# Kernel tuning notes

Measured on AMD Instinct MI355X. Metric: run time of the kernel, lower is better.

Reference implementation:

```python
import jax, jax.numpy as jnp
import numpy as np

NH = 8  # num_heads
CHUNK = 32  # query-block size for chunked L1 cdist


def _mlp(x, w1, b1, w2, b2, w3, b3):
    h = jax.nn.relu(x @ w1 + b1)
    h = jax.nn.relu(h @ w2 + b2)
    return h @ w3 + b3


def _split_heads(x, nh):
    # Faithful to source: reshape last dim as (d, nh) then permute -> [B, nh, S, d]
    B, S, H = x.shape
    return jnp.transpose(x.reshape(B, S, H // nh, nh), (0, 3, 1, 2))


def _cdist_l1(K, Q, chunk=CHUNK):
    # torch.cdist(K, Q, p=1): D[b,h,i,j] = sum_d |K[b,h,i,d] - Q[b,h,j,d]|
    # Chunk over query rows to bound the broadcasted |K-Q| intermediate.
    B, h, Sq, d = Q.shape
    Sk = K.shape[2]
    Qb = jnp.moveaxis(Q.reshape(B, h, Sq // chunk, chunk, d), 2, 0)  # [nb,B,h,chunk,d]

    def block(q):  # q: [B,h,chunk,d]
        return jnp.sum(jnp.abs(K[:, :, :, None, :] - q[:, :, None, :, :]), axis=-1)  # [B,h,Sk,chunk]

    D = jax.lax.map(block, Qb)  # [nb,B,h,Sk,chunk]
    return jnp.moveaxis(D, 0, 3).reshape(B, h, Sk, Sq)


def setup_inputs() -> dict:
    key = jax.random.key(0)
    ks = jax.random.split(key, 32)
    B, S, F, H, O = 4, 1024, 128, 512, 128
    s = 0.02

    def lin(i, fin, fout):
        return (jax.random.normal(ks[i], (fin, fout), jnp.float32) * s,
                jnp.zeros((fout,), jnp.float32))

    inp = {
        'KEY': jax.random.normal(ks[0], (B, S, F), jnp.float32),
        'VALUE': jax.random.normal(ks[1], (B, S, F), jnp.float32),
        'QUERY': jax.random.normal(ks[2], (B, S, F), jnp.float32),
    }
    idx = 3
    for n in ['k', 'q', 'v']:
        for li, (fin, fout) in enumerate([(F, H), (H, H), (H, H)], 1):
            w, b = lin(idx, fin, fout); idx += 1
            inp[f'W{n}_w{li}'] = w
            inp[f'W{n}_b{li}'] = b
    w, b = lin(idx, H, O)
    inp['Wo_w'] = w
    inp['Wo_b'] = b
    return inp


def reference(KEY, VALUE, QUERY,
              Wk_w1, Wk_b1, Wk_w2, Wk_b2, Wk_w3, Wk_b3,
              Wq_w1, Wq_b1, Wq_w2, Wq_b2, Wq_w3, Wq_b3,
              Wv_w1, Wv_b1, Wv_w2, Wv_b2, Wv_w3, Wv_b3,
              Wo_w, Wo_b):
    Wk = _split_heads(_mlp(KEY, Wk_w1, Wk_b1, Wk_w2, Wk_b2, Wk_w3, Wk_b3), NH)   # [B,h,Sk,d]
    Wq = _split_heads(_mlp(QUERY, Wq_w1, Wq_b1, Wq_w2, Wq_b2, Wq_w3, Wq_b3), NH)  # [B,h,Sq,d]
    Wv = _split_heads(_mlp(VALUE, Wv_w1, Wv_b1, Wv_w2, Wv_b2, Wv_w3, Wv_b3), NH)  # [B,h,Sk,d]

    D = _cdist_l1(Wk, Wq)                              # [B,h,Sk,Sq]
    attn = jax.nn.softmax(-(D * D) * 0.5, axis=1)      # softmax over HEAD axis, as in source
    out = jnp.einsum('bhik,bhij->bhjk', attn, Wv)      # [B,h,d,Sq]
    B, h, d, Sq = out.shape
    out = jnp.transpose(out, (0, 2, 1, 3)).reshape(B, d * h, Sq)  # [B,hidden,Sq]
    out = jnp.transpose(out, (0, 2, 1))                # [B,Sq,hidden]
    return out @ Wo_w + Wo_b                           # dropout = identity (eval)
```

## Files before the change

kernel.cpp:

```cpp
#include <hip/hip_runtime.h>
#include <hip/hip_bf16.h>
#include <hip/hip_fp16.h>

typedef unsigned short u16;
typedef __attribute__((ext_vector_type(8))) short short8;
typedef __attribute__((ext_vector_type(4))) float floatx4;

#define DEVI static __device__ __forceinline__

DEVI float bf2f(u16 b) { return __uint_as_float(((unsigned)b) << 16); }
DEVI u16 f2bf(float f) {
  __hip_bfloat16 h = __float2bfloat16(f);
  u16 u; __builtin_memcpy(&u, &h, 2); return u;
}
DEVI u16 f2h(float f) {
  __half h = __float2half(f);
  u16 u; __builtin_memcpy(&u, &h, 2); return u;
}

DEVI void async_ld16(const u16* g, u16* l) {
  __builtin_amdgcn_global_load_lds(
      (const __attribute__((address_space(1))) unsigned int*)g,
      (__attribute__((address_space(3))) unsigned int*)l, 16, 0, 0);
}

template <int CTRL>
DEVI float dpp_add_f(float v) {
  int i; __builtin_memcpy(&i, &v, 4);
  int p = __builtin_amdgcn_update_dpp(0, i, CTRL, 0xF, 0xF, false);
  float pv; __builtin_memcpy(&pv, &p, 4);
  return v + pv;
}

DEVI int hperm(int f) { return ((f & 7) << 6) | (f >> 3); }

struct H4 { __half2 a, b, c, d; };
DEVI H4 toH4(const int4 v) { H4 r; __builtin_memcpy(&r, &v, 16); return r; }
DEVI int4 fromH4(const H4 x) { int4 r; __builtin_memcpy(&r, &x, 16); return r; }

struct TransArgs {
  const float* src[10];
  u16* dst[10];
  int R[10];
  int C[10];
};

__global__ __launch_bounds__(256) void transpose_k(TransArgs t) {
  const int z = blockIdx.z;
  const float* __restrict__ src = t.src[z];
  u16* __restrict__ dst = t.dst[z];
  const int R = t.R[z], C = t.C[z];
  const int c0 = blockIdx.x * 32, r0 = blockIdx.y * 32;
  if (c0 >= C || r0 >= R) return;
  __shared__ float tile[32][33];
  const int tx = threadIdx.x & 31, ty = threadIdx.x >> 5;
  for (int i = ty; i < 32; i += 8)
    tile[i][tx] = src[(size_t)(r0 + i) * C + c0 + tx];
  __syncthreads();
  for (int i = ty; i < 32; i += 8) {
    const int f = r0 + tx;
    const int fi = (z == 9) ? hperm(f) : f;
    dst[(size_t)(c0 + i) * R + fi] = f2bf(tile[tx][i]);
  }
}

struct ConvArgs {
  const float* src[3];
  u16* dst[3];
};

__global__ __launch_bounds__(256) void conv_k(ConvArgs c) {
  const int z = blockIdx.z;
  const float* __restrict__ src = c.src[z];
  u16* __restrict__ dst = c.dst[z];
  const size_t i = ((size_t)blockIdx.x * 256 + threadIdx.x) * 8;
  const float4 f0 = *(const float4*)(src + i);
  const float4 f1 = *(const float4*)(src + i + 4);
  u16 tmp[8] = {f2bf(f0.x), f2bf(f0.y), f2bf(f0.z), f2bf(f0.w),
                f2bf(f1.x), f2bf(f1.y), f2bf(f1.z), f2bf(f1.w)};
  int4 t; __builtin_memcpy(&t, tmp, 16);
  *(int4*)(dst + i) = t;
}

struct GemmArgs {
  const u16* A[3];
  const u16* WT[3];
  const float* bias[3];
  void* C[3];
};

__global__ __launch_bounds__(256, 3) void gemm128(GemmArgs ga, int M, int N, int K,
                                                  int relu, int c_mode, int out_perm) {
  const int z = blockIdx.z;
  const u16* __restrict__ A = ga.A[z];
  const u16* __restrict__ WT = ga.WT[z];
  const float* __restrict__ bias = ga.bias[z];
  void* __restrict__ C = ga.C[z];

  __shared__ u16 As[128 * 64];
  __shared__ u16 Bs[128 * 64];

  const int tid = threadIdx.x;
  const int lane = tid & 63;
  const int wave = tid >> 6;
  const int wm = wave >> 1, wn = wave & 1;
  const int mb = blockIdx.y, nb = blockIdx.x;

  floatx4 acc[4][4];
#pragma unroll
  for (int mi = 0; mi < 4; ++mi)
#pragma unroll
    for (int ni = 0; ni < 4; ++ni) acc[mi][ni] = floatx4{0.f, 0.f, 0.f, 0.f};

  const int g = (lane & 7) ^ ((lane >> 3) & 7);
  const int srow = lane >> 3;
  const size_t aRowBase = (size_t)(mb * 128 + wave * 32 + srow) * K + g * 8;
  const size_t bRowBase = (size_t)(nb * 128 + wave * 32 + srow) * K + g * 8;

  for (int k0 = 0; k0 < K; k0 += 64) {
    __syncthreads();
#pragma unroll
    for (int it = 0; it < 4; ++it) {
      async_ld16(A + aRowBase + (size_t)it * 8 * K + k0, As + (wave * 32 + it * 8) * 64);
      async_ld16(WT + bRowBase + (size_t)it * 8 * K + k0, Bs + (wave * 32 + it * 8) * 64);
    }
    __syncthreads();
#pragma unroll
    for (int ks = 0; ks < 2; ++ks) {
      const int phys = ((ks * 4 + (lane >> 4)) ^ (lane & 7)) * 8;
      short8 af[4], bf[4];
#pragma unroll
      for (int i = 0; i < 4; ++i) {
        const int m = wm * 64 + i * 16 + (lane & 15);
        const int n = wn * 64 + i * 16 + (lane & 15);
        af[i] = *(const short8*)(As + m * 64 + phys);
        bf[i] = *(const short8*)(Bs + n * 64 + phys);
      }
#pragma unroll
      for (int mi = 0; mi < 4; ++mi)
#pragma unroll
        for (int ni = 0; ni < 4; ++ni)
          acc[mi][ni] = __builtin_amdgcn_mfma_f32_16x16x32_bf16(af[mi], bf[ni], acc[mi][ni], 0, 0, 0);
    }
  }

#pragma unroll
  for (int mi = 0; mi < 4; ++mi)
#pragma unroll
    for (int ni = 0; ni < 4; ++ni) {
      const int col = nb * 128 + wn * 64 + ni * 16 + (lane & 15);
      const float bv = bias[col];
      const int colw = out_perm ? hperm(col) : col;
      const floatx4 v = acc[mi][ni];
#pragma unroll
      for (int r = 0; r < 4; ++r) {
        const int row = mb * 128 + wm * 64 + mi * 16 + (lane >> 4) * 4 + r;
        float x = v[r] + bv;
        if (relu) x = fmaxf(x, 0.f);
        if (c_mode == 1)      ((float*)C)[(size_t)row * N + colw] = x;
        else if (c_mode == 2) ((u16*)C)[(size_t)row * N + colw] = f2h(x);
        else                  ((u16*)C)[(size_t)row * N + colw] = f2bf(x);
      }
    }
}

__global__ __launch_bounds__(256, 3) void attn_kernel(const u16* __restrict__ Km,
                                                      const u16* __restrict__ Qm,
                                                      const u16* __restrict__ Vm,
                                                      u16* __restrict__ partial) {
  __shared__ alignas(16) u16 lds[4 * 4096];

  const int tid = threadIdx.x;
  const int lane = tid & 63;
  const int wave = tid >> 6;
  const int wid = blockIdx.x * 4 + wave;
  const int qt = wid & 63;
  const int sp = (wid >> 6) & 15;
  const int b = wid >> 10;
  const int j0 = qt * 16;

  const int qg = lane >> 4;
  const int h = (lane >> 1) & 7;
  const int half = lane & 1;

  int grans[4];
#pragma unroll
  for (int pi = 0; pi < 4; ++pi)
    grans[pi] = h * 8 + half * 4 + ((pi + h) & 3);

  H4 Qh[4][4];
#pragma unroll
  for (int qi = 0; qi < 4; ++qi) {
    const u16* qrow = Qm + (size_t)(b * 1024 + j0 + qg + qi * 4) * 512;
#pragma unroll
    for (int pi = 0; pi < 4; ++pi)
      Qh[qi][pi] = toH4(*(const int4*)(qrow + grans[pi] * 8));
  }

  const __half2 z2 = __float2half2_rn(0.f);
  H4 o[4][4];
#pragma unroll
  for (int qi = 0; qi < 4; ++qi)
#pragma unroll
    for (int pi = 0; pi < 4; ++pi) { o[qi][pi].a = z2; o[qi][pi].b = z2; o[qi][pi].c = z2; o[qi][pi].d = z2; }

  const int keyBase = b * 1024 + sp * 64;
  const u16* kgb = Km + (size_t)keyBase * 512 + lane * 8;
  const u16* vgb = Vm + (size_t)keyBase * 512 + lane * 8;
  u16* wbase = lds + wave * 4096;

  async_ld16(kgb, wbase);
  async_ld16(kgb + 512, wbase + 512);
  async_ld16(vgb, wbase + 1024);
  async_ld16(vgb + 512, wbase + 1536);

#pragma unroll 1
  for (int cc = 0; cc < 32; ++cc) {
    asm volatile("s_waitcnt vmcnt(0)" ::: "memory");
    __builtin_amdgcn_sched_barrier(0);
    const int cur = cc & 1;
    const u16* buf = wbase + cur * 2048;
    if (cc < 31) {
      const u16* kg = kgb + (size_t)(cc + 1) * 1024;
      const u16* vg = vgb + (size_t)(cc + 1) * 1024;
      u16* nb = wbase + (cur ^ 1) * 2048;
      async_ld16(kg, nb);
      async_ld16(kg + 512, nb + 512);
      async_ld16(vg, nb + 1024);
      async_ld16(vg + 512, nb + 1536);
    }

#pragma unroll
    for (int r = 0; r < 2; ++r) {
      const u16* krow = buf + r * 512;
      const u16* vrow = buf + 1024 + r * 512;

      __half2 a0[4], a1[4];
#pragma unroll
      for (int qi = 0; qi < 4; ++qi) { a0[qi] = z2; a1[qi] = z2; }
#pragma unroll
      for (int pi = 0; pi < 4; ++pi) {
        const H4 k4 = toH4(*(const int4*)(krow + grans[pi] * 8));
#pragma unroll
        for (int qi = 0; qi < 4; ++qi) {
          a0[qi] = __hadd2(a0[qi], __habs2(__hsub2(k4.a, Qh[qi][pi].a)));
          a1[qi] = __hadd2(a1[qi], __habs2(__hsub2(k4.b, Qh[qi][pi].b)));
          a0[qi] = __hadd2(a0[qi], __habs2(__hsub2(k4.c, Qh[qi][pi].c)));
          a1[qi] = __hadd2(a1[qi], __habs2(__hsub2(k4.d, Qh[qi][pi].d)));
        }
      }

      __half2 wh[4];
#pragma unroll
      for (int qi = 0; qi < 4; ++qi) {
        const __half2 s2 = __hadd2(a0[qi], a1[qi]);
        float d8p = __half2float(__low2half(s2)) + __half2float(__high2half(s2));
        const float d8 = dpp_add_f<0xB1>(d8p);
        const float e = __expf(-0.5f * d8 * d8);
        float nrm = e;
        nrm = dpp_add_f<0x4E>(nrm);
        nrm = dpp_add_f<0x141>(nrm);
        nrm = dpp_add_f<0x140>(nrm);
        const float w = e * __builtin_amdgcn_rcpf(nrm);
        wh[qi] = __float2half2_rn(w);
      }

#pragma unroll
      for (int pi = 0; pi < 4; ++pi) {
        const H4 v4 = toH4(*(const int4*)(vrow + grans[pi] * 8));
#pragma unroll
        for (int qi = 0; qi < 4; ++qi) {
          o[qi][pi].a = __hfma2(wh[qi], v4.a, o[qi][pi].a);
          o[qi][pi].b = __hfma2(wh[qi], v4.b, o[qi][pi].b);
          o[qi][pi].c = __hfma2(wh[qi], v4.c, o[qi][pi].c);
          o[qi][pi].d = __hfma2(wh[qi], v4.d, o[qi][pi].d);
        }
      }
    }
  }

  u16* Ew = wbase;
#pragma unroll
  for (int qi = 0; qi < 4; ++qi) {
#pragma unroll
    for (int pi = 0; pi < 4; ++pi)
      *(int4*)(Ew + qg * 512 + grans[pi] * 8) = fromH4(o[qi][pi]);
    asm volatile("s_waitcnt lgkmcnt(0)" ::: "memory");
#pragma unroll
    for (int p = 0; p < 4; ++p) {
      const int4 v = *(const int4*)(Ew + p * 512 + lane * 8);
      u16* dst = partial + (size_t)sp * (4096 * 512) + (size_t)(b * 1024 + j0 + p + qi * 4) * 512;
      *(int4*)(dst + lane * 8) = v;
    }
    asm volatile("s_waitcnt lgkmcnt(0)" ::: "memory");
  }
}

__global__ __launch_bounds__(256) void reduce_k(const u16* __restrict__ p,
                                                u16* __restrict__ out) {
  const size_t i = ((size_t)blockIdx.x * 256 + threadIdx.x) * 8;
  float s[8] = {0.f, 0.f, 0.f, 0.f, 0.f, 0.f, 0.f, 0.f};
#pragma unroll
  for (int sp = 0; sp < 16; ++sp) {
    const int4 t = *(const int4*)(p + (size_t)sp * (4096 * 512) + i);
    const __half* th = reinterpret_cast<const __half*>(&t);
#pragma unroll
    for (int j = 0; j < 8; ++j) s[j] += __half2float(th[j]);
  }
  int4 pk;
  u16* pu = reinterpret_cast<u16*>(&pk);
#pragma unroll
  for (int j = 0; j < 8; ++j) pu[j] = f2bf(s[j]);
  *(int4*)(out + i) = pk;
}

extern "C" void kernel_launch(void* const* d_in, const int* in_sizes, int n_in,
                              void* d_out, int out_size, void* d_ws, size_t ws_size,
                              hipStream_t stream) {
  (void)in_sizes; (void)n_in; (void)out_size; (void)ws_size;
  char* wsp = (char*)d_ws;
  size_t off = 0;
  auto take = [&](size_t bytes) {
    void* p = (void*)(wsp + off);
    off += ((bytes + 255) & ~(size_t)255);
    return p;
  };

  static const int wR[10] = {128, 512, 512, 128, 512, 512, 128, 512, 512, 512};
  static const int wC[10] = {512, 512, 512, 512, 512, 512, 512, 512, 512, 128};
  static const int widx[10] = {3, 5, 7, 9, 11, 13, 15, 17, 19, 21};

  u16* WT[10];
  for (int i = 0; i < 10; ++i) WT[i] = (u16*)take((size_t)wR[i] * wC[i] * 2);
  u16* a0[3]; for (int i = 0; i < 3; ++i) a0[i] = (u16*)take((size_t)4096 * 128 * 2);
  u16* h1[3]; for (int i = 0; i < 3; ++i) h1[i] = (u16*)take((size_t)4096 * 512 * 2);
  u16* h2[3]; for (int i = 0; i < 3; ++i) h2[i] = (u16*)take((size_t)4096 * 512 * 2);
  u16* partial = (u16*)take((size_t)16 * 4096 * 512 * 2);

  TransArgs ta;
  for (int i = 0; i < 10; ++i) {
    ta.src[i] = (const float*)d_in[widx[i]];
    ta.dst[i] = WT[i];
    ta.R[i] = wR[i];
    ta.C[i] = wC[i];
  }
  hipLaunchKernelGGL(transpose_k, dim3(16, 16, 10), dim3(256), 0, stream, ta);

  ConvArgs ca;
  ca.src[0] = (const float*)d_in[0]; ca.src[1] = (const float*)d_in[2]; ca.src[2] = (const float*)d_in[1];
  ca.dst[0] = a0[0]; ca.dst[1] = a0[1]; ca.dst[2] = a0[2];
  hipLaunchKernelGGL(conv_k, dim3(256, 1, 3), dim3(256), 0, stream, ca);

  GemmArgs g1 = {};
  for (int i = 0; i < 3; ++i) g1.A[i] = a0[i];
  g1.WT[0] = WT[0]; g1.WT[1] = WT[3]; g1.WT[2] = WT[6];
  g1.bias[0] = (const float*)d_in[4]; g1.bias[1] = (const float*)d_in[10]; g1.bias[2] = (const float*)d_in[16];
  g1.C[0] = h1[0]; g1.C[1] = h1[1]; g1.C[2] = h1[2];
  hipLaunchKernelGGL(gemm128, dim3(4, 32, 3), dim3(256), 0, stream, g1, 4096, 512, 128, 1, 0, 0);

  GemmArgs g2 = {};
  for (int i = 0; i < 3; ++i) { g2.A[i] = h1[i]; g2.C[i] = h2[i]; }
  g2.WT[0] = WT[1]; g2.WT[1] = WT[4]; g2.WT[2] = WT[7];
  g2.bias[0] = (const float*)d_in[6]; g2.bias[1] = (const float*)d_in[12]; g2.bias[2] = (const float*)d_in[18];
  hipLaunchKernelGGL(gemm128, dim3(4, 32, 3), dim3(256), 0, stream, g2, 4096, 512, 512, 1, 0, 0);

  GemmArgs g3 = {};
  for (int i = 0; i < 3; ++i) { g3.A[i] = h2[i]; g3.C[i] = (void*)h1[i]; }
  g3.WT[0] = WT[2]; g3.WT[1] = WT[5]; g3.WT[2] = WT[8];
  g3.bias[0] = (const float*)d_in[8]; g3.bias[1] = (const float*)d_in[14]; g3.bias[2] = (const float*)d_in[20];
  hipLaunchKernelGGL(gemm128, dim3(4, 32, 3), dim3(256), 0, stream, g3, 4096, 512, 512, 0, 2, 1);

  hipLaunchKernelGGL(attn_kernel, dim3(1024), dim3(256), 0, stream, h1[0], h1[1], h1[2], partial);

  hipLaunchKernelGGL(reduce_k, dim3(1024), dim3(256), 0, stream, partial, h2[0]);

  GemmArgs g4 = {};
  g4.A[0] = h2[0]; g4.WT[0] = WT[9]; g4.bias[0] = (const float*)d_in[22]; g4.C[0] = d_out;
  hipLaunchKernelGGL(gemm128, dim3(1, 32, 1), dim3(256), 0, stream, g4, 4096, 128, 512, 0, 1, 0);
}
```

Measured before the change: 357.4 us.

## Fuse split-K partial reduction into final output GEMM with atomic accumulation

The separate reduce kernel and the final 4096x512x128 GEMM are replaced by one kernel. Each block reduces the 16 fp16 partial slices for its 128x64 A-tile straight into LDS as bf16 and multiplies it against a 64-wide K chunk of the output weights. Results are accumulated into a zeroed fp32 output with atomicAdd across 8 K-chunks, and bias is added only by the first chunk. This removes the intermediate bf16 round trip through global memory and one launch, and spreads the final GEMM over 256 blocks instead of 32. In exchange it adds a memset, fp32 atomics on the output, and a summation order that is no longer deterministic.

```diff
diff --git a/kernel.cpp b/kernel.cpp
--- a/kernel.cpp
+++ b/kernel.cpp
@@ -296,22 +296,85 @@
   }
 }
 
-__global__ __launch_bounds__(256) void reduce_k(const u16* __restrict__ p,
-                                                u16* __restrict__ out) {
-  const size_t i = ((size_t)blockIdx.x * 256 + threadIdx.x) * 8;
-  float s[8] = {0.f, 0.f, 0.f, 0.f, 0.f, 0.f, 0.f, 0.f};
-#pragma unroll
-  for (int sp = 0; sp < 16; ++sp) {
-    const int4 t = *(const int4*)(p + (size_t)sp * (4096 * 512) + i);
-    const __half* th = reinterpret_cast<const __half*>(&t);
-#pragma unroll
-    for (int j = 0; j < 8; ++j) s[j] += __half2float(th[j]);
-  }
-  int4 pk;
-  u16* pu = reinterpret_cast<u16*>(&pk);
-#pragma unroll
-  for (int j = 0; j < 8; ++j) pu[j] = f2bf(s[j]);
-  *(int4*)(out + i) = pk;
+__global__ __launch_bounds__(256, 3) void gemm_final(const u16* __restrict__ P,
+                                                     const u16* __restrict__ WT9,
+                                                     const float* __restrict__ bias,
+                                                     float* __restrict__ out) {
+  __shared__ u16 As[128 * 64];
+  __shared__ u16 Bs[128 * 64];
+
+  const int tid = threadIdx.x;
+  const int lane = tid & 63;
+  const int wave = tid >> 6;
+  const int wm = wave >> 1, wn = wave & 1;
+  const int mb = blockIdx.y;
+  const int kc = blockIdx.x;
+  const int k0 = kc * 64;
+
+  const int g = (lane & 7) ^ ((lane >> 3) & 7);
+  const int srow = lane >> 3;
+
+  const size_t bRowBase = (size_t)(wave * 32 + srow) * 512 + g * 8;
+#pragma unroll
+  for (int it = 0; it < 4; ++it)
+    async_ld16(WT9 + bRowBase + (size_t)it * 8 * 512 + k0, Bs + (wave * 32 + it * 8) * 64);
+
+#pragma unroll
+  for (int it = 0; it < 4; ++it) {
+    const size_t gaddr = (size_t)(mb * 128 + wave * 32 + it * 8 + srow) * 512 + k0 + g * 8;
+    float s[8] = {0.f, 0.f, 0.f, 0.f, 0.f, 0.f, 0.f, 0.f};
+#pragma unroll
+    for (int sp = 0; sp < 16; ++sp) {
+      const int4 t = *(const int4*)(P + (size_t)sp * (4096 * 512) + gaddr);
+      const __half* th = reinterpret_cast<const __half*>(&t);
+#pragma unroll
+      for (int j = 0; j < 8; ++j) s[j] += __half2float(th[j]);
+    }
+    u16 tmp[8];
+#pragma unroll
+    for (int j = 0; j < 8; ++j) tmp[j] = f2bf(s[j]);
+    int4 pk; __builtin_memcpy(&pk, tmp, 16);
+    *(int4*)(As + (wave * 32 + it * 8) * 64 + lane * 8) = pk;
+  }
+  __syncthreads();
+
+  floatx4 acc[4][4];
+#pragma unroll
+  for (int mi = 0; mi < 4; ++mi)
+#pragma unroll
+    for (int ni = 0; ni < 4; ++ni) acc[mi][ni] = floatx4{0.f, 0.f, 0.f, 0.f};
+
+#pragma unroll
+  for (int ks = 0; ks < 2; ++ks) {
+    const int phys = ((ks * 4 + (lane >> 4)) ^ (lane & 7)) * 8;
+    short8 af[4], bf[4];
+#pragma unroll
+    for (int i = 0; i < 4; ++i) {
+      const int m = wm * 64 + i * 16 + (lane & 15);
+      const int n = wn * 64 + i * 16 + (lane & 15);
+      af[i] = *(const short8*)(As + m * 64 + phys);
+      bf[i] = *(const short8*)(Bs + n * 64 + phys);
+    }
+#pragma unroll
+    for (int mi = 0; mi < 4; ++mi)
+#pragma unroll
+      for (int ni = 0; ni < 4; ++ni)
+        acc[mi][ni] = __builtin_amdgcn_mfma_f32_16x16x32_bf16(af[mi], bf[ni], acc[mi][ni], 0, 0, 0);
+  }
+
+#pragma unroll
+  for (int mi = 0; mi < 4; ++mi)
+#pragma unroll
+    for (int ni = 0; ni < 4; ++ni) {
+      const int col = wn * 64 + ni * 16 + (lane & 15);
+      const float bv = (kc == 0) ? bias[col] : 0.f;
+      const floatx4 v = acc[mi][ni];
+#pragma unroll
+      for (int r = 0; r < 4; ++r) {
+        const int row = mb * 128 + wm * 64 + mi * 16 + (lane >> 4) * 4 + r;
+        atomicAdd(&out[(size_t)row * 128 + col], v[r] + bv);
+      }
+    }
 }
 
 extern "C" void kernel_launch(void* const* d_in, const int* in_sizes, int n_in,
@@ -372,9 +435,7 @@
 
   hipLaunchKernelGGL(attn_kernel, dim3(1024), dim3(256), 0, stream, h1[0], h1[1], h1[2], partial);
 
-  hipLaunchKernelGGL(reduce_k, dim3(1024), dim3(256), 0, stream, partial, h2[0]);
-
-  GemmArgs g4 = {};
-  g4.A[0] = h2[0]; g4.WT[0] = WT[9]; g4.bias[0] = (const float*)d_in[22]; g4.C[0] = d_out;
-  hipLaunchKernelGGL(gemm128, dim3(1, 32, 1), dim3(256), 0, stream, g4, 4096, 128, 512, 0, 1, 0);
-}
+  hipMemsetAsync(d_out, 0, (size_t)4096 * 128 * sizeof(float), stream);
+  hipLaunchKernelGGL(gemm_final, dim3(8, 32), dim3(256), 0, stream,
+                     partial, WT[9], (const float*)d_in[22], (float*)d_out);
+}
```

Measured after the change: 356.9 us, median of 2. No clear change (-0.1%).
